# Kernel tuning notes

Hardware: AMD Instinct MI355X
Metric: run time of the kernel (lower is better)

The kernel has to match this reference:

```python
import jax, jax.numpy as jnp
import numpy as np

B, S, H = 8, 1024, 1024
NH, DH = 16, 64
F_DIM, E, TOPK = 4096, 8, 2
EPS = 1e-5


def setup_inputs() -> dict:
    key = jax.random.key(0)
    ks = jax.random.split(key, 12)
    s = 0.02
    return {
        "x": jax.random.normal(ks[0], (B, S, H), jnp.float32),
        "ln1_w": jnp.ones((H,), jnp.float32),
        "ln1_b": jnp.zeros((H,), jnp.float32),
        "ln2_w": jnp.ones((H,), jnp.float32),
        "ln2_b": jnp.zeros((H,), jnp.float32),
        "in_proj_w": jax.random.normal(ks[1], (3 * H, H), jnp.float32) * s,
        "in_proj_b": jnp.zeros((3 * H,), jnp.float32),
        "out_proj_w": jax.random.normal(ks[2], (H, H), jnp.float32) * s,
        "out_proj_b": jnp.zeros((H,), jnp.float32),
        "gate_w": jax.random.normal(ks[3], (E, H), jnp.float32) * s,
        "gate_b": jnp.zeros((E,), jnp.float32),
        "w1": jax.random.normal(ks[4], (E, H, F_DIM), jnp.float32) * s,
        "b1": jnp.zeros((E, F_DIM), jnp.float32),
        "w2": jax.random.normal(ks[5], (E, F_DIM, H), jnp.float32) * s,
        "b2": jnp.zeros((E, H), jnp.float32),
    }


def _layernorm(x, w, b):
    mu = jnp.mean(x, axis=-1, keepdims=True)
    var = jnp.var(x, axis=-1, keepdims=True)
    return (x - mu) * jax.lax.rsqrt(var + EPS) * w + b


def reference(x, ln1_w, ln1_b, ln2_w, ln2_b, in_proj_w, in_proj_b,
              out_proj_w, out_proj_b, gate_w, gate_b, w1, b1, w2, b2):
    # --- attention sub-block ---
    xn = _layernorm(x, ln1_w, ln1_b)
    qkv = xn @ in_proj_w.T + in_proj_b                     # [B,S,3H]
    q, k, v = jnp.split(qkv, 3, axis=-1)
    q = q.reshape(B, S, NH, DH).transpose(0, 2, 1, 3)      # [B,NH,S,DH]
    k = k.reshape(B, S, NH, DH).transpose(0, 2, 1, 3)
    v = v.reshape(B, S, NH, DH).transpose(0, 2, 1, 3)
    scores = jnp.einsum("bhqd,bhkd->bhqk", q, k) / jnp.sqrt(jnp.float32(DH))
    attn = jax.nn.softmax(scores, axis=-1)
    ctx = jnp.einsum("bhqk,bhkd->bhqd", attn, v)
    ctx = ctx.transpose(0, 2, 1, 3).reshape(B, S, H)
    x = x + ctx @ out_proj_w.T + out_proj_b

    # --- MoE sub-block (dense compute-all-experts, top-k combine) ---
    xn2 = _layernorm(x, ln2_w, ln2_b)
    logits = xn2 @ gate_w.T + gate_b                       # [B,S,E]
    topk_vals, topk_idx = jax.lax.top_k(logits, TOPK)      # [B,S,K]
    probs = jax.nn.softmax(topk_vals, axis=-1)
    hid = jax.nn.gelu(jnp.einsum("bsh,ehf->bsef", xn2, w1) + b1, approximate=False)
    expert_out = jnp.einsum("bsef,efh->bseh", hid, w2) + b2  # [B,S,E,H]
    selected = jnp.take_along_axis(expert_out, topk_idx[..., None], axis=2)  # [B,S,K,H]
    moe_out = jnp.sum(probs[..., None] * selected, axis=2)
    return x + moe_out
```

## Files before the change

### kernel.cpp

```cpp
#include <hip/hip_runtime.h>
#include <math.h>

typedef unsigned short u16;
typedef short short8 __attribute__((ext_vector_type(8)));
typedef float f32x4 __attribute__((ext_vector_type(4)));
typedef unsigned short us4 __attribute__((ext_vector_type(4)));

#define NTOK 8192
#define NEXP 8

__device__ __forceinline__ u16 f2bf(float f) {
  union { float f; unsigned u; } v; v.f = f;
  unsigned r = v.u + 0x7FFFu + ((v.u >> 16) & 1u);
  return (u16)(r >> 16);
}
__device__ __forceinline__ float bf2f(u16 u) {
  union { unsigned u; float f; } v; v.u = ((unsigned)u) << 16; return v.f;
}
__device__ __forceinline__ void gload16(const u16* src, u16* ldsDst) {
  __builtin_amdgcn_global_load_lds(
    (const __attribute__((address_space(1))) unsigned int*)(const void*)src,
    (__attribute__((address_space(3))) unsigned int*)(void*)ldsDst, 16, 0, 0);
}
__device__ __forceinline__ float gelu_f(float v) {
  float ax = fabsf(v) * 0.70710678f;
  float t = __builtin_amdgcn_rcpf(1.0f + 0.3275911f * ax);
  float p = t * (0.254829592f + t * (-0.284496736f + t * (1.421413741f +
            t * (-1.453152027f + t * 1.061405429f))));
  float er = 1.0f - p * __expf(-ax * ax);
  er = copysignf(er, v);
  return 0.5f * v * (1.0f + er);
}

__global__ void cast_kernel(const float* __restrict__ in, u16* __restrict__ out, int n4) {
  int i = blockIdx.x * blockDim.x + threadIdx.x;
  if (i < n4) {
    float4 v = ((const float4*)in)[i];
    us4 o;
    o[0] = f2bf(v.x); o[1] = f2bf(v.y); o[2] = f2bf(v.z); o[3] = f2bf(v.w);
    ((us4*)out)[i] = o;
  }
}

__global__ void transpose_cast(const float* __restrict__ in, u16* __restrict__ out, int R, int C) {
  __shared__ float tile[64][65];
  const size_t eoff = (size_t)blockIdx.z * (size_t)R * (size_t)C;
  in += eoff; out += eoff;
  const int rb = blockIdx.y * 64, cb = blockIdx.x * 64;
  const int tid = threadIdx.x;
  const int lr4 = tid >> 4;
  const int lc4 = (tid & 15) * 4;
#pragma unroll
  for (int p = 0; p < 4; ++p) {
    float4 v = *(const float4*)&in[(size_t)(rb + p * 16 + lr4) * C + cb + lc4];
    tile[p * 16 + lr4][lc4 + 0] = v.x;
    tile[p * 16 + lr4][lc4 + 1] = v.y;
    tile[p * 16 + lr4][lc4 + 2] = v.z;
    tile[p * 16 + lr4][lc4 + 3] = v.w;
  }
  __syncthreads();
  const int oc = tid >> 3;
  const int orr = (tid & 7) * 8;
#pragma unroll
  for (int p = 0; p < 2; ++p) {
    int c = p * 32 + oc;
    short8 o;
#pragma unroll
    for (int j = 0; j < 8; ++j) o[j] = (short)f2bf(tile[orr + j][c]);
    *(short8*)&out[(size_t)(cb + c) * R + rb + orr] = o;
  }
}

__global__ void ln1_kernel(const float* __restrict__ x, const float* __restrict__ w,
                           const float* __restrict__ b, u16* __restrict__ xn) {
  const int t = blockIdx.x, tid = threadIdx.x;
  __shared__ float red[8];
  float4 v = ((const float4*)(x + (size_t)t * 1024))[tid];
  float s  = v.x + v.y + v.z + v.w;
  float sq = v.x*v.x + v.y*v.y + v.z*v.z + v.w*v.w;
#pragma unroll
  for (int m = 1; m < 64; m <<= 1) { s += __shfl_xor(s, m, 64); sq += __shfl_xor(sq, m, 64); }
  if ((tid & 63) == 0) { red[tid >> 6] = s; red[4 + (tid >> 6)] = sq; }
  __syncthreads();
  float S = red[0] + red[1] + red[2] + red[3];
  float Q = red[4] + red[5] + red[6] + red[7];
  float mu  = S * (1.0f / 1024.0f);
  float var = Q * (1.0f / 1024.0f) - mu * mu;
  float inv = rsqrtf(var + 1e-5f);
  float4 wv = ((const float4*)w)[tid];
  float4 bv = ((const float4*)b)[tid];
  us4 o;
  o[0] = f2bf((v.x - mu) * inv * wv.x + bv.x);
  o[1] = f2bf((v.y - mu) * inv * wv.y + bv.y);
  o[2] = f2bf((v.z - mu) * inv * wv.z + bv.z);
  o[3] = f2bf((v.w - mu) * inv * wv.w + bv.w);
  ((us4*)(xn + (size_t)t * 1024))[tid] = o;
}

__global__ void ln2_gate_kernel(const float* __restrict__ x2, const float* __restrict__ w,
                                const float* __restrict__ b, const float* __restrict__ gw,
                                const float* __restrict__ gb, u16* __restrict__ xn2,
                                int* __restrict__ cnt, int* __restrict__ list_tok,
                                float* __restrict__ list_prob, int* __restrict__ tok2slot) {
  const int t = blockIdx.x, tid = threadIdx.x;
  __shared__ float red[8];
  __shared__ float logits[NEXP];
  __shared__ float xrow[1024];
  float4 v = ((const float4*)(x2 + (size_t)t * 1024))[tid];
  float s  = v.x + v.y + v.z + v.w;
  float sq = v.x*v.x + v.y*v.y + v.z*v.z + v.w*v.w;
#pragma unroll
  for (int m = 1; m < 64; m <<= 1) { s += __shfl_xor(s, m, 64); sq += __shfl_xor(sq, m, 64); }
  if ((tid & 63) == 0) { red[tid >> 6] = s; red[4 + (tid >> 6)] = sq; }
  __syncthreads();
  float S = red[0] + red[1] + red[2] + red[3];
  float Q = red[4] + red[5] + red[6] + red[7];
  float mu  = S * (1.0f / 1024.0f);
  float var = Q * (1.0f / 1024.0f) - mu * mu;
  float inv = rsqrtf(var + 1e-5f);
  float4 wv = ((const float4*)w)[tid];
  float4 bv = ((const float4*)b)[tid];
  float n0 = (v.x - mu) * inv * wv.x + bv.x;
  float n1 = (v.y - mu) * inv * wv.y + bv.y;
  float n2 = (v.z - mu) * inv * wv.z + bv.z;
  float n3 = (v.w - mu) * inv * wv.w + bv.w;
  xrow[tid*4+0] = n0; xrow[tid*4+1] = n1; xrow[tid*4+2] = n2; xrow[tid*4+3] = n3;
  us4 o; o[0] = f2bf(n0); o[1] = f2bf(n1); o[2] = f2bf(n2); o[3] = f2bf(n3);
  ((us4*)(xn2 + (size_t)t * 1024))[tid] = o;
  __syncthreads();
  int e = tid >> 5, l32 = tid & 31;
  const float* gwe = gw + e * 1024;
  float part = 0.0f;
  for (int i = l32; i < 1024; i += 32) part += xrow[i] * gwe[i];
#pragma unroll
  for (int m = 1; m < 32; m <<= 1) part += __shfl_xor(part, m, 64);
  if (l32 == 0) logits[e] = part + gb[e];
  __syncthreads();
  if (tid == 0) {
    float v0 = -1e30f; int e0 = 0;
#pragma unroll
    for (int i = 0; i < NEXP; ++i) { float L = logits[i]; if (L > v0) { v0 = L; e0 = i; } }
    float v1 = -1e30f; int e1 = 0;
#pragma unroll
    for (int i = 0; i < NEXP; ++i) { if (i == e0) continue; float L = logits[i]; if (L > v1) { v1 = L; e1 = i; } }
    float texp = expf(v1 - v0);
    float p0 = 1.0f / (1.0f + texp);
    float p1 = texp / (1.0f + texp);
    int s0 = atomicAdd(&cnt[e0], 1);
    list_tok[e0 * NTOK + s0] = t; list_prob[e0 * NTOK + s0] = p0;
    int s1 = atomicAdd(&cnt[e1], 1);
    list_tok[e1 * NTOK + s1] = t; list_prob[e1 * NTOK + s1] = p1;
    if (tok2slot) {
      tok2slot[2 * t]     = e0 * NTOK + s0;
      tok2slot[2 * t + 1] = e1 * NTOK + s1;
    }
  }
}

__global__ void plan_kernel(const int* __restrict__ cnt, int* __restrict__ meta) {
  if (threadIdx.x == 0) {
    int base = 0, p = 0;
    for (int e = 0; e < NEXP; ++e) {
      meta[e] = base;
      int c = cnt[e];
      base += c;
      int nm = (c + 127) >> 7;
      for (int i = 0; i < nm; ++i) { meta[16 + 2 * p] = e; meta[17 + 2 * p] = i << 7; ++p; }
    }
    meta[8] = p;
  }
}

__global__ void xgather_kernel(const u16* __restrict__ xn2, const int* __restrict__ meta,
                               const int* __restrict__ tok2slot, u16* __restrict__ xg) {
  const int t = blockIdx.x, tid = threadIdx.x;
  short8 v = ((const short8*)(xn2 + (size_t)t * 1024))[tid];
  int c0 = tok2slot[2 * t], c1 = tok2slot[2 * t + 1];
  int g0 = meta[c0 >> 13] + (c0 & 8191);
  int g1 = meta[c1 >> 13] + (c1 & 8191);
  ((short8*)(xg + (size_t)g0 * 1024))[tid] = v;
  ((short8*)(xg + (size_t)g1 * 1024))[tid] = v;
}

__launch_bounds__(256)
__global__ void attn_kernel(const u16* __restrict__ qkv, u16* __restrict__ ctx) {
  const int bh = blockIdx.y;
  const int b = bh >> 4, h = bh & 15;
  const int q0 = blockIdx.x * 64;
  const int tokBase = b * 1024;
  __shared__ __align__(16) u16 Qs[64 * 72];
  __shared__ __align__(16) u16 Ks[64 * 72];
  __shared__ __align__(16) u16 Vts[64 * 72];
  __shared__ __align__(16) u16 Ps[64 * 72];
  const int tid = threadIdx.x;
  const int wave = tid >> 6, lane = tid & 63, g = lane >> 4, lr = lane & 15;

  {
    int r = tid >> 2, d0 = (tid & 3) * 16;
    const u16* src = qkv + (size_t)(tokBase + q0 + r) * 3072 + h * 64 + d0;
    *(short8*)&Qs[r * 72 + d0]     = *(const short8*)src;
    *(short8*)&Qs[r * 72 + d0 + 8] = *(const short8*)(src + 8);
  }
  __syncthreads();
  short8 aq0 = *(const short8*)&Qs[(wave * 16 + lr) * 72 + g * 8];
  short8 aq1 = *(const short8*)&Qs[(wave * 16 + lr) * 72 + 32 + g * 8];

  const f32x4 zf = {0.f, 0.f, 0.f, 0.f};
  f32x4 Ofr[4] = {zf, zf, zf, zf};
  float m_run[4], l_run[4];
#pragma unroll
  for (int r = 0; r < 4; ++r) { m_run[r] = -1e30f; l_run[r] = 0.f; }

  for (int kt = 0; kt < 1024; kt += 64) {
    __syncthreads();
    {
      int r = tid >> 2, d0 = (tid & 3) * 16;
      const u16* ksrc = qkv + (size_t)(tokBase + kt + r) * 3072 + 1024 + h * 64 + d0;
      *(short8*)&Ks[r * 72 + d0]     = *(const short8*)ksrc;
      *(short8*)&Ks[r * 72 + d0 + 8] = *(const short8*)(ksrc + 8);
      const u16* vsrc = qkv + (size_t)(tokBase + kt + r) * 3072 + 2048 + h * 64 + d0;
      short8 v0 = *(const short8*)vsrc, v1 = *(const short8*)(vsrc + 8);
#pragma unroll
      for (int j = 0; j < 8; ++j) Vts[(d0 + j) * 72 + r] = (u16)v0[j];
#pragma unroll
      for (int j = 0; j < 8; ++j) Vts[(d0 + 8 + j) * 72 + r] = (u16)v1[j];
    }
    __syncthreads();
    f32x4 sf[4];
#pragma unroll
    for (int n = 0; n < 4; ++n) sf[n] = zf;
#pragma unroll
    for (int n = 0; n < 4; ++n) {
      short8 bk0 = *(const short8*)&Ks[(n * 16 + lr) * 72 + g * 8];
      short8 bk1 = *(const short8*)&Ks[(n * 16 + lr) * 72 + 32 + g * 8];
      sf[n] = __builtin_amdgcn_mfma_f32_16x16x32_bf16(aq0, bk0, sf[n], 0, 0, 0);
      sf[n] = __builtin_amdgcn_mfma_f32_16x16x32_bf16(aq1, bk1, sf[n], 0, 0, 0);
    }
#pragma unroll
    for (int n = 0; n < 4; ++n)
#pragma unroll
      for (int r = 0; r < 4; ++r) sf[n][r] *= 0.125f;
    float mnew[4], sc[4];
#pragma unroll
    for (int r = 0; r < 4; ++r) {
      float t0 = fmaxf(fmaxf(sf[0][r], sf[1][r]), fmaxf(sf[2][r], sf[3][r]));
#pragma unroll
      for (int msk = 1; msk < 16; msk <<= 1) t0 = fmaxf(t0, __shfl_xor(t0, msk, 64));
      mnew[r] = fmaxf(m_run[r], t0);
      sc[r] = __expf(m_run[r] - mnew[r]);
      m_run[r] = mnew[r];
    }
#pragma unroll
    for (int n = 0; n < 4; ++n)
#pragma unroll
      for (int r = 0; r < 4; ++r) sf[n][r] = __expf(sf[n][r] - mnew[r]);
#pragma unroll
    for (int r = 0; r < 4; ++r) {
      float s0 = sf[0][r] + sf[1][r] + sf[2][r] + sf[3][r];
#pragma unroll
      for (int msk = 1; msk < 16; msk <<= 1) s0 += __shfl_xor(s0, msk, 64);
      l_run[r] = l_run[r] * sc[r] + s0;
    }
#pragma unroll
    for (int nd = 0; nd < 4; ++nd)
#pragma unroll
      for (int r = 0; r < 4; ++r) Ofr[nd][r] *= sc[r];
#pragma unroll
    for (int n = 0; n < 4; ++n)
#pragma unroll
      for (int r = 0; r < 4; ++r)
        Ps[(wave * 16 + g * 4 + r) * 72 + n * 16 + lr] = f2bf(sf[n][r]);
    __syncthreads();
    short8 ap0 = *(const short8*)&Ps[(wave * 16 + lr) * 72 + g * 8];
    short8 ap1 = *(const short8*)&Ps[(wave * 16 + lr) * 72 + 32 + g * 8];
#pragma unroll
    for (int nd = 0; nd < 4; ++nd) {
      short8 bv0 = *(const short8*)&Vts[(nd * 16 + lr) * 72 + g * 8];
      short8 bv1 = *(const short8*)&Vts[(nd * 16 + lr) * 72 + 32 + g * 8];
      Ofr[nd] = __builtin_amdgcn_mfma_f32_16x16x32_bf16(ap0, bv0, Ofr[nd], 0, 0, 0);
      Ofr[nd] = __builtin_amdgcn_mfma_f32_16x16x32_bf16(ap1, bv1, Ofr[nd], 0, 0, 0);
    }
  }
#pragma unroll
  for (int nd = 0; nd < 4; ++nd)
#pragma unroll
    for (int r = 0; r < 4; ++r) {
      int tok = tokBase + q0 + wave * 16 + g * 4 + r;
      int col = h * 64 + nd * 16 + lr;
      ctx[(size_t)tok * 1024 + col] = f2bf(Ofr[nd][r] / l_run[r]);
    }
}

template<int EPI>
__launch_bounds__(256, 2)
__global__ void gemmP(const u16* __restrict__ Abase, const u16* __restrict__ Bbase,
                      int K, int lda, int N, int ldc, int nSlotsFixed,
                      const float* __restrict__ bias,
                      const float* __restrict__ resid,
                      float* __restrict__ outF,
                      u16* __restrict__ outB,
                      const int* __restrict__ cnt,
                      const int* __restrict__ meta,
                      const int* __restrict__ list_tok,
                      const float* __restrict__ list_prob) {
  const int gx = gridDim.x, G = gridDim.y;
  const int nwg = gx * G;
  int orig = blockIdx.y + blockIdx.x * G;
  int q8 = nwg >> 3, r8 = nwg & 7, xcd = orig & 7, lid = orig >> 3;
  int wg = (xcd < r8 ? xcd * (q8 + 1) : r8 * (q8 + 1) + (xcd - r8) * q8) + lid;
  const int bx = wg / G, gidx = wg % G;
  const int n0 = bx * 128;

  const int S = (EPI >= 2) ? meta[8] : nSlotsFixed;
  if (gidx >= S) return;
  const int nslots = (S - gidx + G - 1) / G;
  const int NT = K >> 6;
  const int ntLog = 31 - __builtin_clz((unsigned)NT);
  const int nIt = nslots << ntLog;

  __shared__ __align__(16) u16 As[2][8192];
  __shared__ __align__(16) u16 Bs[2][8192];

  const int tid = threadIdx.x;
  const int wave = tid >> 6, lane = tid & 63, gp = lane >> 4, lr = lane & 15;
  const int wm = wave >> 1, wn = wave & 1;

  unsigned boff[4];
#pragma unroll
  for (int i = 0; i < 4; ++i) {
    int ci = i * 256 + tid;
    int row = ci >> 3, c = ci & 7;
    int lc = c ^ (row & 7);
    boff[i] = (unsigned)(n0 + row) * (unsigned)K + (unsigned)(lc << 3);
  }

  int eC, m0C, MC, sbC; const u16* BwC; unsigned aoffC[4];
  int eN, m0N, MN, sbN; const u16* BwN; unsigned aoffN[4];

  auto loadSlot = [&](int s, int& e, int& m0, int& M, int& sb, const u16*& Bw, unsigned (&ao)[4]) {
    if constexpr (EPI >= 2) {
      e = meta[16 + 2 * s]; m0 = meta[17 + 2 * s]; M = cnt[e]; sb = meta[e];
      Bw = Bbase + (size_t)e * (size_t)N * (size_t)K;
    } else {
      e = 0; m0 = s * 128; M = NTOK; sb = 0; Bw = Bbase;
    }
#pragma unroll
    for (int i = 0; i < 4; ++i) {
      int ci = i * 256 + tid;
      int row = ci >> 3, c = ci & 7;
      int lc = c ^ (row & 7);
      int arow;
      if constexpr (EPI == 2) {
        int r = m0 + row; if (r > M - 1) r = M - 1;
        arow = list_tok[e * NTOK + r];
      } else if constexpr (EPI >= 3) {
        int r = m0 + row; if (r > M - 1) r = M - 1;
        arow = sb + r;
      } else {
        arow = m0 + row;
      }
      ao[i] = (unsigned)arow * (unsigned)lda + (unsigned)(lc << 3);
    }
  };

  loadSlot(gidx, eC, m0C, MC, sbC, BwC, aoffC);
  if (nslots > 1) loadSlot(gidx + G, eN, m0N, MN, sbN, BwN, aoffN);
  else { eN = eC; m0N = m0C; MN = MC; sbN = sbC; BwN = BwC;
#pragma unroll
         for (int i = 0; i < 4; ++i) aoffN[i] = aoffC[i]; }

  const int sw = lr & 7;
  const int arb = (wm * 64 + lr) * 64;
  const int brb = (wn * 64 + lr) * 64;
  const int sk0 = (gp ^ sw) * 8;
  const int sk1 = ((4 + gp) ^ sw) * 8;

  const f32x4 zf = {0.f, 0.f, 0.f, 0.f};
  f32x4 acc[4][4];
#pragma unroll
  for (int m = 0; m < 4; ++m)
#pragma unroll
    for (int n = 0; n < 4; ++n) acc[m][n] = zf;

#pragma unroll
  for (int i = 0; i < 4; ++i) {
    gload16(Abase + aoffC[i], &As[0][(i * 256 + wave * 64) << 3]);
    gload16(BwC + boff[i], &Bs[0][(i * 256 + wave * 64) << 3]);
  }
  asm volatile("" ::: "memory");
#pragma unroll
  for (int i = 0; i < 4; ++i) {
    gload16(Abase + aoffC[i] + 64, &As[1][(i * 256 + wave * 64) << 3]);
    gload16(BwC + boff[i] + 64, &Bs[1][(i * 256 + wave * 64) << 3]);
  }
  asm volatile("s_waitcnt vmcnt(8)" ::: "memory");
  __builtin_amdgcn_s_barrier();

  for (int it = 0; it < nIt; ++it) {
    const int sRel = it >> ntLog;
    const u16* Ab = As[it & 1];
    const u16* Bb = Bs[it & 1];
    short8 af[4][2], bf[4][2];
#pragma unroll
    for (int m = 0; m < 4; ++m) {
      af[m][0] = *(const short8*)&Ab[arb + m * 1024 + sk0];
      af[m][1] = *(const short8*)&Ab[arb + m * 1024 + sk1];
    }
#pragma unroll
    for (int n = 0; n < 4; ++n) {
      bf[n][0] = *(const short8*)&Bb[brb + n * 1024 + sk0];
      bf[n][1] = *(const short8*)&Bb[brb + n * 1024 + sk1];
    }
    asm volatile("s_waitcnt lgkmcnt(0)" ::: "memory");
    __builtin_amdgcn_s_barrier();
    {
      int it2 = it + 2;
      if (it2 < nIt) {
        bool nx = (it2 >> ntLog) != sRel;
        int kt2 = (it2 & (NT - 1)) << 6;
        int b2 = it2 & 1;
        const u16* bw = nx ? BwN : BwC;
#pragma unroll
        for (int i = 0; i < 4; ++i) {
          unsigned ao = nx ? aoffN[i] : aoffC[i];
          gload16(Abase + ao + kt2, &As[b2][(i * 256 + wave * 64) << 3]);
          gload16(bw + boff[i] + kt2, &Bs[b2][(i * 256 + wave * 64) << 3]);
        }
      }
    }
    __builtin_amdgcn_s_setprio(1);
#pragma unroll
    for (int kk = 0; kk < 2; ++kk)
#pragma unroll
      for (int m = 0; m < 4; ++m)
#pragma unroll
        for (int n = 0; n < 4; ++n)
          acc[m][n] = __builtin_amdgcn_mfma_f32_16x16x32_bf16(af[m][kk], bf[n][kk], acc[m][n], 0, 0, 0);
    __builtin_amdgcn_s_setprio(0);
    if (it < nIt - 3) { asm volatile("s_waitcnt vmcnt(8)" ::: "memory"); }
    else              { asm volatile("s_waitcnt vmcnt(0)" ::: "memory"); }
    __builtin_amdgcn_s_barrier();

    if ((it & (NT - 1)) == NT - 1) {
#pragma unroll
      for (int m = 0; m < 4; ++m) {
        int rloc = wm * 64 + m * 16 + gp * 4;
#pragma unroll
        for (int n = 0; n < 4; ++n) {
          int gc = n0 + wn * 64 + n * 16 + lr;
          float bcol;
          if constexpr (EPI >= 2) bcol = bias[(size_t)eC * N + gc];
          else bcol = bias[gc];
#pragma unroll
          for (int r = 0; r < 4; ++r) {
            int ridx = m0C + rloc + r;
            float vv = acc[m][n][r] + bcol;
            if constexpr (EPI == 0) {
              outB[(size_t)ridx * ldc + gc] = f2bf(vv);
            } else if constexpr (EPI == 1) {
              size_t off = (size_t)ridx * ldc + gc;
              outF[off] = vv + resid[off];
            } else if constexpr (EPI == 2 || EPI == 5) {
              if (ridx < MC)
                outB[(size_t)(sbC + ridx) * ldc + gc] = f2bf(gelu_f(vv));
            } else if constexpr (EPI == 3) {
              if (ridx < MC)
                outB[(size_t)(sbC + ridx) * ldc + gc] = f2bf(vv);
            } else {
              if (ridx < MC) {
                int tok = list_tok[eC * NTOK + ridx];
                float p = list_prob[eC * NTOK + ridx];
                atomicAdd(&outF[(size_t)tok * ldc + gc], vv * p);
              }
            }
            acc[m][n][r] = 0.f;
          }
        }
      }
      eC = eN; m0C = m0N; MC = MN; sbC = sbN; BwC = BwN;
#pragma unroll
      for (int i = 0; i < 4; ++i) aoffC[i] = aoffN[i];
      int s2 = gidx + (sRel + 2) * G;
      if (s2 < S) loadSlot(s2, eN, m0N, MN, sbN, BwN, aoffN);
    }
  }
}

__global__ void combine_kernel(const u16* __restrict__ part, const int* __restrict__ cnt,
                               const int* __restrict__ tok2slot, const float* __restrict__ lprb,
                               float* __restrict__ out) {
  const int t = blockIdx.x, tid = threadIdx.x;
  __shared__ int base[NEXP];
  if (tid == 0) {
    int b = 0;
#pragma unroll
    for (int j = 0; j < NEXP; ++j) { base[j] = b; b += cnt[j]; }
  }
  __syncthreads();
  int c0 = tok2slot[2 * t], c1 = tok2slot[2 * t + 1];
  float p0 = lprb[c0], p1 = lprb[c1];
  int g0 = base[c0 >> 13] + (c0 & 8191);
  int g1 = base[c1 >> 13] + (c1 & 8191);
  us4 a = ((const us4*)(part + (size_t)g0 * 1024))[tid];
  us4 b = ((const us4*)(part + (size_t)g1 * 1024))[tid];
  float4 o = ((const float4*)(out + (size_t)t * 1024))[tid];
  o.x += p0 * bf2f(a[0]) + p1 * bf2f(b[0]);
  o.y += p0 * bf2f(a[1]) + p1 * bf2f(b[1]);
  o.z += p0 * bf2f(a[2]) + p1 * bf2f(b[2]);
  o.w += p0 * bf2f(a[3]) + p1 * bf2f(b[3]);
  ((float4*)(out + (size_t)t * 1024))[tid] = o;
}

extern "C" void kernel_launch(void* const* d_in, const int* in_sizes, int n_in,
                              void* d_out, int out_size, void* d_ws, size_t ws_size,
                              hipStream_t stream) {
  const float* x    = (const float*)d_in[0];
  const float* ln1w = (const float*)d_in[1];
  const float* ln1b = (const float*)d_in[2];
  const float* ln2w = (const float*)d_in[3];
  const float* ln2b = (const float*)d_in[4];
  const float* inw  = (const float*)d_in[5];
  const float* inb  = (const float*)d_in[6];
  const float* outw = (const float*)d_in[7];
  const float* outb = (const float*)d_in[8];
  const float* gw   = (const float*)d_in[9];
  const float* gb   = (const float*)d_in[10];
  const float* w1   = (const float*)d_in[11];
  const float* b1   = (const float*)d_in[12];
  const float* w2   = (const float*)d_in[13];
  const float* b2   = (const float*)d_in[14];
  float* out = (float*)d_out;
  char* ws = (char*)d_ws;

  u16* xn1 = (u16*)(ws + 0);
  u16* qkv = (u16*)(ws + 16777216);
  u16* ctx = (u16*)(ws + 67108864);
  u16* hid = (u16*)(ws + 0);
  u16* w1t = (u16*)(ws + 134217728);
  u16* winb  = (u16*)(ws + 218103808);
  u16* woutb = (u16*)(ws + 224395264);
  u16* w2t = (u16*)(ws + 134217728);
  u16* xg   = (u16*)(ws + 201326592);
  u16* part = (u16*)(ws + 201326592);

  const bool bigWS = ws_size >= 235475456ull;
  u16* xn2 = bigWS ? (u16*)(ws + 0)
                   : (u16*)(ws + 201326592);
  int *cnt, *meta, *ltok, *t2s; float* lprb;
  if (bigWS) {
    cnt  = (int*)(ws + 234881024);
    meta = (int*)(ws + 234883072);
    ltok = (int*)(ws + 234887168);
    lprb = (float*)(ws + 235149312);
    t2s  = (int*)(ws + 235411456);
  } else {
    cnt  = (int*)(ws + 226492416);
    meta = (int*)(ws + 226494464);
    ltok = (int*)(ws + 226498560);
    lprb = (float*)(ws + 226760704);
    t2s  = nullptr;
  }

  cast_kernel<<<3072, 256, 0, stream>>>(inw, winb, 786432);
  cast_kernel<<<1024, 256, 0, stream>>>(outw, woutb, 262144);
  transpose_cast<<<dim3(64, 16, 8), 256, 0, stream>>>(w1, w1t, 1024, 4096);

  ln1_kernel<<<8192, 256, 0, stream>>>(x, ln1w, ln1b, xn1);
  gemmP<0><<<dim3(24, 16), 256, 0, stream>>>(xn1, winb, 1024, 1024, 3072, 3072, 64,
      inb, nullptr, nullptr, qkv, nullptr, nullptr, nullptr, nullptr);
  attn_kernel<<<dim3(16, 128), 256, 0, stream>>>(qkv, ctx);
  gemmP<1><<<dim3(8, 32), 256, 0, stream>>>(ctx, woutb, 1024, 1024, 1024, 1024, 64,
      outb, x, out, nullptr, nullptr, nullptr, nullptr, nullptr);

  hipMemsetAsync(cnt, 0, 32, stream);
  ln2_gate_kernel<<<8192, 256, 0, stream>>>(out, ln2w, ln2b, gw, gb, xn2, cnt, ltok, lprb, t2s);
  plan_kernel<<<1, 64, 0, stream>>>(cnt, meta);
  if (bigWS) {
    xgather_kernel<<<8192, 128, 0, stream>>>(xn2, meta, t2s, xg);
    gemmP<5><<<dim3(32, 16), 256, 0, stream>>>(xg, w1t, 1024, 1024, 4096, 4096, 0,
        b1, nullptr, nullptr, hid, cnt, meta, ltok, lprb);
  } else {
    gemmP<2><<<dim3(32, 16), 256, 0, stream>>>(xn2, w1t, 1024, 1024, 4096, 4096, 0,
        b1, nullptr, nullptr, hid, cnt, meta, ltok, lprb);
  }
  transpose_cast<<<dim3(16, 64, 8), 256, 0, stream>>>(w2, w2t, 4096, 1024);
  if (bigWS) {
    gemmP<3><<<dim3(8, 64), 256, 0, stream>>>(hid, w2t, 4096, 4096, 1024, 1024, 0,
        b2, nullptr, nullptr, part, cnt, meta, ltok, lprb);
    combine_kernel<<<8192, 256, 0, stream>>>(part, cnt, t2s, lprb, out);
  } else {
    gemmP<4><<<dim3(8, 64), 256, 0, stream>>>(hid, w2t, 4096, 4096, 1024, 1024, 0,
        b2, nullptr, out, nullptr, cnt, meta, ltok, lprb);
  }
}
```

Baseline: 1.090 ms.

## Double query rows per attention block and retune GEMM grid sizes

Each attention workgroup now handles 128 query rows instead of 64, with every wave processing two 16-row halves. Each K/V tile loaded into shared memory is therefore reused across twice as many queries, halving K/V global traffic and the transpose work per query. The grid y-dimension of the QKV and out-projection GEMMs is also changed, presumably to match how gemmP splits work across the grid. The cost is more registers and shared memory per block and half as many attention blocks, which may lower occupancy.

```diff
diff --git a/kernel.cpp b/kernel.cpp
--- a/kernel.cpp
+++ b/kernel.cpp
@@ -186,30 +186,37 @@
 __global__ void attn_kernel(const u16* __restrict__ qkv, u16* __restrict__ ctx) {
   const int bh = blockIdx.y;
   const int b = bh >> 4, h = bh & 15;
-  const int q0 = blockIdx.x * 64;
+  const int q0 = blockIdx.x * 128;
   const int tokBase = b * 1024;
-  __shared__ __align__(16) u16 Qs[64 * 72];
+  __shared__ __align__(16) u16 Qs[128 * 72];
   __shared__ __align__(16) u16 Ks[64 * 72];
   __shared__ __align__(16) u16 Vts[64 * 72];
-  __shared__ __align__(16) u16 Ps[64 * 72];
+  __shared__ __align__(16) u16 Ps[128 * 72];
   const int tid = threadIdx.x;
   const int wave = tid >> 6, lane = tid & 63, g = lane >> 4, lr = lane & 15;
 
-  {
+#pragma unroll
+  for (int hf = 0; hf < 2; ++hf) {
     int r = tid >> 2, d0 = (tid & 3) * 16;
-    const u16* src = qkv + (size_t)(tokBase + q0 + r) * 3072 + h * 64 + d0;
-    *(short8*)&Qs[r * 72 + d0]     = *(const short8*)src;
-    *(short8*)&Qs[r * 72 + d0 + 8] = *(const short8*)(src + 8);
+    const u16* src = qkv + (size_t)(tokBase + q0 + hf * 64 + r) * 3072 + h * 64 + d0;
+    *(short8*)&Qs[(hf * 64 + r) * 72 + d0]     = *(const short8*)src;
+    *(short8*)&Qs[(hf * 64 + r) * 72 + d0 + 8] = *(const short8*)(src + 8);
   }
   __syncthreads();
-  short8 aq0 = *(const short8*)&Qs[(wave * 16 + lr) * 72 + g * 8];
-  short8 aq1 = *(const short8*)&Qs[(wave * 16 + lr) * 72 + 32 + g * 8];
+  short8 aq[2][2];
+#pragma unroll
+  for (int hf = 0; hf < 2; ++hf) {
+    aq[hf][0] = *(const short8*)&Qs[(hf * 64 + wave * 16 + lr) * 72 + g * 8];
+    aq[hf][1] = *(const short8*)&Qs[(hf * 64 + wave * 16 + lr) * 72 + 32 + g * 8];
+  }
 
   const f32x4 zf = {0.f, 0.f, 0.f, 0.f};
-  f32x4 Ofr[4] = {zf, zf, zf, zf};
-  float m_run[4], l_run[4];
-#pragma unroll
-  for (int r = 0; r < 4; ++r) { m_run[r] = -1e30f; l_run[r] = 0.f; }
+  f32x4 Ofr[2][4];
+  float m_run[2][4], l_run[2][4];
+#pragma unroll
+  for (int hf = 0; hf < 2; ++hf)
+#pragma unroll
+    for (int r = 0; r < 4; ++r) { Ofr[hf][r] = zf; m_run[hf][r] = -1e30f; l_run[hf][r] = 0.f; }
 
   for (int kt = 0; kt < 1024; kt += 64) {
     __syncthreads();
@@ -226,69 +233,77 @@
       for (int j = 0; j < 8; ++j) Vts[(d0 + 8 + j) * 72 + r] = (u16)v1[j];
     }
     __syncthreads();
-    f32x4 sf[4];
-#pragma unroll
-    for (int n = 0; n < 4; ++n) sf[n] = zf;
-#pragma unroll
-    for (int n = 0; n < 4; ++n) {
-      short8 bk0 = *(const short8*)&Ks[(n * 16 + lr) * 72 + g * 8];
-      short8 bk1 = *(const short8*)&Ks[(n * 16 + lr) * 72 + 32 + g * 8];
-      sf[n] = __builtin_amdgcn_mfma_f32_16x16x32_bf16(aq0, bk0, sf[n], 0, 0, 0);
-      sf[n] = __builtin_amdgcn_mfma_f32_16x16x32_bf16(aq1, bk1, sf[n], 0, 0, 0);
-    }
-#pragma unroll
-    for (int n = 0; n < 4; ++n)
-#pragma unroll
-      for (int r = 0; r < 4; ++r) sf[n][r] *= 0.125f;
-    float mnew[4], sc[4];
-#pragma unroll
-    for (int r = 0; r < 4; ++r) {
-      float t0 = fmaxf(fmaxf(sf[0][r], sf[1][r]), fmaxf(sf[2][r], sf[3][r]));
-#pragma unroll
-      for (int msk = 1; msk < 16; msk <<= 1) t0 = fmaxf(t0, __shfl_xor(t0, msk, 64));
-      mnew[r] = fmaxf(m_run[r], t0);
-      sc[r] = __expf(m_run[r] - mnew[r]);
-      m_run[r] = mnew[r];
-    }
-#pragma unroll
-    for (int n = 0; n < 4; ++n)
-#pragma unroll
-      for (int r = 0; r < 4; ++r) sf[n][r] = __expf(sf[n][r] - mnew[r]);
-#pragma unroll
-    for (int r = 0; r < 4; ++r) {
-      float s0 = sf[0][r] + sf[1][r] + sf[2][r] + sf[3][r];
-#pragma unroll
-      for (int msk = 1; msk < 16; msk <<= 1) s0 += __shfl_xor(s0, msk, 64);
-      l_run[r] = l_run[r] * sc[r] + s0;
-    }
+#pragma unroll
+    for (int hf = 0; hf < 2; ++hf) {
+      f32x4 sf[4];
+#pragma unroll
+      for (int n = 0; n < 4; ++n) sf[n] = zf;
+#pragma unroll
+      for (int n = 0; n < 4; ++n) {
+        short8 bk0 = *(const short8*)&Ks[(n * 16 + lr) * 72 + g * 8];
+        short8 bk1 = *(const short8*)&Ks[(n * 16 + lr) * 72 + 32 + g * 8];
+        sf[n] = __builtin_amdgcn_mfma_f32_16x16x32_bf16(aq[hf][0], bk0, sf[n], 0, 0, 0);
+        sf[n] = __builtin_amdgcn_mfma_f32_16x16x32_bf16(aq[hf][1], bk1, sf[n], 0, 0, 0);
+      }
+#pragma unroll
+      for (int n = 0; n < 4; ++n)
+#pragma unroll
+        for (int r = 0; r < 4; ++r) sf[n][r] *= 0.125f;
+      float mnew[4], sc[4];
+#pragma unroll
+      for (int r = 0; r < 4; ++r) {
+        float t0 = fmaxf(fmaxf(sf[0][r], sf[1][r]), fmaxf(sf[2][r], sf[3][r]));
+#pragma unroll
+        for (int msk = 1; msk < 16; msk <<= 1) t0 = fmaxf(t0, __shfl_xor(t0, msk, 64));
+        mnew[r] = fmaxf(m_run[hf][r], t0);
+        sc[r] = __expf(m_run[hf][r] - mnew[r]);
+        m_run[hf][r] = mnew[r];
+      }
+#pragma unroll
+      for (int n = 0; n < 4; ++n)
+#pragma unroll
+        for (int r = 0; r < 4; ++r) sf[n][r] = __expf(sf[n][r] - mnew[r]);
+#pragma unroll
+      for (int r = 0; r < 4; ++r) {
+        float s0 = sf[0][r] + sf[1][r] + sf[2][r] + sf[3][r];
+#pragma unroll
+        for (int msk = 1; msk < 16; msk <<= 1) s0 += __shfl_xor(s0, msk, 64);
+        l_run[hf][r] = l_run[hf][r] * sc[r] + s0;
+      }
+#pragma unroll
+      for (int nd = 0; nd < 4; ++nd)
+#pragma unroll
+        for (int r = 0; r < 4; ++r) Ofr[hf][nd][r] *= sc[r];
+#pragma unroll
+      for (int n = 0; n < 4; ++n)
+#pragma unroll
+        for (int r = 0; r < 4; ++r)
+          Ps[(hf * 64 + wave * 16 + g * 4 + r) * 72 + n * 16 + lr] = f2bf(sf[n][r]);
+    }
+    __syncthreads();
+#pragma unroll
+    for (int hf = 0; hf < 2; ++hf) {
+      short8 ap0 = *(const short8*)&Ps[(hf * 64 + wave * 16 + lr) * 72 + g * 8];
+      short8 ap1 = *(const short8*)&Ps[(hf * 64 + wave * 16 + lr) * 72 + 32 + g * 8];
+#pragma unroll
+      for (int nd = 0; nd < 4; ++nd) {
+        short8 bv0 = *(const short8*)&Vts[(nd * 16 + lr) * 72 + g * 8];
+        short8 bv1 = *(const short8*)&Vts[(nd * 16 + lr) * 72 + 32 + g * 8];
+        Ofr[hf][nd] = __builtin_amdgcn_mfma_f32_16x16x32_bf16(ap0, bv0, Ofr[hf][nd], 0, 0, 0);
+        Ofr[hf][nd] = __builtin_amdgcn_mfma_f32_16x16x32_bf16(ap1, bv1, Ofr[hf][nd], 0, 0, 0);
+      }
+    }
+  }
+#pragma unroll
+  for (int hf = 0; hf < 2; ++hf)
 #pragma unroll
     for (int nd = 0; nd < 4; ++nd)
 #pragma unroll
-      for (int r = 0; r < 4; ++r) Ofr[nd][r] *= sc[r];
-#pragma unroll
-    for (int n = 0; n < 4; ++n)
-#pragma unroll
-      for (int r = 0; r < 4; ++r)
-        Ps[(wave * 16 + g * 4 + r) * 72 + n * 16 + lr] = f2bf(sf[n][r]);
-    __syncthreads();
-    short8 ap0 = *(const short8*)&Ps[(wave * 16 + lr) * 72 + g * 8];
-    short8 ap1 = *(const short8*)&Ps[(wave * 16 + lr) * 72 + 32 + g * 8];
-#pragma unroll
-    for (int nd = 0; nd < 4; ++nd) {
-      short8 bv0 = *(const short8*)&Vts[(nd * 16 + lr) * 72 + g * 8];
-      short8 bv1 = *(const short8*)&Vts[(nd * 16 + lr) * 72 + 32 + g * 8];
-      Ofr[nd] = __builtin_amdgcn_mfma_f32_16x16x32_bf16(ap0, bv0, Ofr[nd], 0, 0, 0);
-      Ofr[nd] = __builtin_amdgcn_mfma_f32_16x16x32_bf16(ap1, bv1, Ofr[nd], 0, 0, 0);
-    }
-  }
-#pragma unroll
-  for (int nd = 0; nd < 4; ++nd)
-#pragma unroll
-    for (int r = 0; r < 4; ++r) {
-      int tok = tokBase + q0 + wave * 16 + g * 4 + r;
-      int col = h * 64 + nd * 16 + lr;
-      ctx[(size_t)tok * 1024 + col] = f2bf(Ofr[nd][r] / l_run[r]);
-    }
+      for (int r = 0; r < 4; ++r) {
+        int tok = tokBase + q0 + hf * 64 + wave * 16 + g * 4 + r;
+        int col = h * 64 + nd * 16 + lr;
+        ctx[(size_t)tok * 1024 + col] = f2bf(Ofr[hf][nd][r] / l_run[hf][r]);
+      }
 }
 
 template<int EPI>
@@ -566,10 +581,10 @@
   transpose_cast<<<dim3(64, 16, 8), 256, 0, stream>>>(w1, w1t, 1024, 4096);
 
   ln1_kernel<<<8192, 256, 0, stream>>>(x, ln1w, ln1b, xn1);
-  gemmP<0><<<dim3(24, 16), 256, 0, stream>>>(xn1, winb, 1024, 1024, 3072, 3072, 64,
+  gemmP<0><<<dim3(24, 21), 256, 0, stream>>>(xn1, winb, 1024, 1024, 3072, 3072, 64,
       inb, nullptr, nullptr, qkv, nullptr, nullptr, nullptr, nullptr);
-  attn_kernel<<<dim3(16, 128), 256, 0, stream>>>(qkv, ctx);
-  gemmP<1><<<dim3(8, 32), 256, 0, stream>>>(ctx, woutb, 1024, 1024, 1024, 1024, 64,
+  attn_kernel<<<dim3(8, 128), 256, 0, stream>>>(qkv, ctx);
+  gemmP<1><<<dim3(8, 64), 256, 0, stream>>>(ctx, woutb, 1024, 1024, 1024, 1024, 64,
       outb, x, out, nullptr, nullptr, nullptr, nullptr, nullptr);
 
   hipMemsetAsync(cnt, 0, 32, stream);
```

Result: no change. 1.092 ms (+0.2%).
